# Kernel optimization log

Measured on AMD Instinct MI355X. Metric: run time of the kernel, lower is better.

The kernel has to match this reference:

```python
import jax, jax.numpy as jnp
import numpy as np

EMBED_DIM = 1024
NUM_HEADS = 16
HEAD_DIM = EMBED_DIM // NUM_HEADS


def setup_inputs() -> dict:
    key = jax.random.key(0)
    ks = jax.random.split(key, 11)
    B, S, D = 4, 2048, EMBED_DIM
    s = 1.0 / np.sqrt(D)
    return {
        "query": jax.random.normal(ks[0], (B, S, D), jnp.float32),
        "key": jax.random.normal(ks[1], (B, S, D), jnp.float32),
        "value": jax.random.normal(ks[2], (B, S, D), jnp.float32),
        "Wq": jax.random.normal(ks[3], (D, D), jnp.float32) * s,
        "bq": jnp.zeros((D,), jnp.float32),
        "Wk": jax.random.normal(ks[4], (D, D), jnp.float32) * s,
        "bk": jnp.zeros((D,), jnp.float32),
        "Wv": jax.random.normal(ks[5], (D, D), jnp.float32) * s,
        "bv": jnp.zeros((D,), jnp.float32),
        "Wo": jax.random.normal(ks[6], (D, D), jnp.float32) * s,
        "bo": jnp.zeros((D,), jnp.float32),
    }


def _split_heads(x):
    B, S, D = x.shape
    return x.reshape(B, S, NUM_HEADS, HEAD_DIM).transpose(0, 2, 1, 3)  # (B,H,S,hd)


def reference(query, key, value, Wq, bq, Wk, bk, Wv, bv, Wo, bo):
    q = _split_heads(query @ Wq + bq)
    k = _split_heads(key @ Wk + bk)
    v = _split_heads(value @ Wv + bv)
    # naive scaled dot-product attention: full (B,H,S,S) scores materialized
    scores = jnp.einsum("bhqd,bhkd->bhqk", q, k) / np.sqrt(HEAD_DIM).astype(np.float32)
    attn = jax.nn.softmax(scores, axis=-1)
    ctx = jnp.einsum("bhqk,bhkd->bhqd", attn, v)
    B, H, S, hd = ctx.shape
    ctx = ctx.transpose(0, 2, 1, 3).reshape(B, S, H * hd)
    return ctx @ Wo + bo
```

## Files before the change

### kernel.cpp

```cpp
#include <hip/hip_runtime.h>

typedef unsigned short u16;
typedef unsigned int u32;
typedef _Float16 f16;
typedef __attribute__((ext_vector_type(8))) _Float16 f16x8;
typedef __attribute__((ext_vector_type(4))) float f32x4;
typedef __attribute__((ext_vector_type(4))) u32 u32x4;
typedef __attribute__((ext_vector_type(2))) u32 u32x2;
typedef __attribute__((ext_vector_type(4))) u16 u16x4;

static __device__ __forceinline__ u16 f16r(float f) {
  return __builtin_bit_cast(u16, (_Float16)f);
}
static __device__ __forceinline__ u32 packh(float a, float b) {
  return __builtin_bit_cast(u32, __builtin_amdgcn_cvt_pkrtz(a, b));
}
static __device__ __forceinline__ void gload16(const u16* g, u16* l) {
  __builtin_amdgcn_global_load_lds((const __attribute__((address_space(1))) void*)g,
                                   (__attribute__((address_space(3))) void*)l, 16, 0, 0);
}
static __device__ __forceinline__ void gload16f(const float* g, float* l) {
  __builtin_amdgcn_global_load_lds((const __attribute__((address_space(1))) void*)g,
                                   (__attribute__((address_space(3))) void*)l, 16, 0, 0);
}

__global__ __launch_bounds__(256) void wtrans4_k(
    const float* __restrict__ Wq, const float* __restrict__ Wk,
    const float* __restrict__ Wv, const float* __restrict__ Wo,
    u16* __restrict__ Tq, u16* __restrict__ Tk, u16* __restrict__ Tv, u16* __restrict__ To) {
  int z = blockIdx.z;
  const float* W = z == 0 ? Wq : z == 1 ? Wk : z == 2 ? Wv : Wo;
  u16* WT = z == 0 ? Tq : z == 1 ? Tk : z == 2 ? Tv : To;
  __shared__ float tile[32][33];
  int k0 = blockIdx.x * 32, n0 = blockIdx.y * 32;
  int t = threadIdx.x;
  int r = t >> 3, c = (t & 7) * 4;
  f32x4 v = *(const f32x4*)&W[(size_t)(k0 + r) * 1024 + n0 + c];
  tile[r][c + 0] = v[0]; tile[r][c + 1] = v[1]; tile[r][c + 2] = v[2]; tile[r][c + 3] = v[3];
  __syncthreads();
  int n = n0 + (t >> 3), kbase = k0 + (t & 7) * 4;
  u16x4 o;
#pragma unroll
  for (int j = 0; j < 4; j++) o[j] = f16r(tile[(t & 7) * 4 + j][t >> 3]);
  int nt = n >> 7, row = n & 127;
  int kt = kbase >> 5, lc = (kbase >> 3) & 3, e = kbase & 7;
  int pc = lc ^ ((row >> 1) & 3);
  *(u16x4*)&WT[((size_t)(nt * 32 + kt) * 128 + row) * 32 + pc * 8 + e] = o;
}

__global__ __launch_bounds__(256) void gemm_qkv_k(
    const float* __restrict__ Aq, const float* __restrict__ Ak, const float* __restrict__ Av,
    const u16* __restrict__ Tq, const u16* __restrict__ Tk, const u16* __restrict__ Tv,
    const float* __restrict__ bq, const float* __restrict__ bk, const float* __restrict__ bv,
    u16* __restrict__ Qo, u16* __restrict__ Ko, u16* __restrict__ Vo, float qscale) {
  int z = blockIdx.z;
  const float* A = z == 0 ? Aq : z == 1 ? Ak : Av;
  const u16* BT = z == 0 ? Tq : z == 1 ? Tk : Tv;
  const float* bias = z == 0 ? bq : z == 1 ? bk : bv;
  u16* out = z == 0 ? Qo : z == 1 ? Ko : Vo;
  int vmode = (z == 2);
  float scale = z == 0 ? qscale : 1.0f;

  __shared__ float As[2][128 * 32];
  __shared__ u16 Bs[2][128 * 32];
  int lid = blockIdx.x;
  int xcd = lid & 7, idx = lid >> 3;
  int bx = idx & 7, by = xcd * 8 + (idx >> 3);
  int n0 = bx * 128, m0 = by * 128;
  int tid = threadIdx.x, lane = tid & 63;
  int w = tid >> 6, wr = w >> 1, wc = w & 1;
  int fq = lane & 15, fc = lane >> 4;
  f32x4 acc[4][4] = {};
  const u16* BTb = BT + (size_t)bx * 131072;

  auto stage = [&](int ks, int sel) {
    const float* Ab = A + (size_t)m0 * 1024 + ks * 32;
#pragma unroll
    for (int i = 0; i < 4; i++) {
      int u = (w * 4 + i) * 64 + lane;
      int row = u >> 3, pc = u & 7;
      int koff = (pc ^ (row & 7)) << 2;
      gload16f(Ab + (size_t)row * 1024 + koff, &As[sel][(w * 4 + i) * 256]);
    }
    const u16* Bt = BTb + ks * 4096;
#pragma unroll
    for (int i = 0; i < 2; i++)
      gload16(Bt + (w * 2 + i) * 512 + lane * 8, &Bs[sel][(w * 2 + i) * 512]);
  };

  stage(0, 0);
  stage(1, 1);
  for (int ks = 0; ks < 32; ks++) {
    int cur = ks & 1;
    if (ks < 31) asm volatile("s_waitcnt vmcnt(6)" ::: "memory");
    else         asm volatile("s_waitcnt vmcnt(0)" ::: "memory");
    __builtin_amdgcn_s_barrier();
    __builtin_amdgcn_sched_barrier(0);
    f16x8 af[4], bfv[4];
#pragma unroll
    for (int mi = 0; mi < 4; mi++) {
      int row = wr * 64 + mi * 16 + fq;
      int pc0 = (2 * fc) ^ (row & 7);
      f32x4 x0 = *(const f32x4*)&As[cur][row * 32 + pc0 * 4];
      f32x4 x1 = *(const f32x4*)&As[cur][row * 32 + (pc0 ^ 1) * 4];
      u32x4 pk = {packh(x0[0], x0[1]), packh(x0[2], x0[3]),
                  packh(x1[0], x1[1]), packh(x1[2], x1[3])};
      af[mi] = __builtin_bit_cast(f16x8, pk);
    }
#pragma unroll
    for (int ni = 0; ni < 4; ni++) {
      int row = wc * 64 + ni * 16 + fq;
      bfv[ni] = *(const f16x8*)&Bs[cur][row * 32 + (fc ^ ((row >> 1) & 3)) * 8];
    }
    __builtin_amdgcn_s_setprio(1);
#pragma unroll
    for (int mi = 0; mi < 4; mi++)
#pragma unroll
      for (int ni = 0; ni < 4; ni++)
        acc[mi][ni] = __builtin_amdgcn_mfma_f32_16x16x32_f16(af[mi], bfv[ni], acc[mi][ni], 0, 0, 0);
    __builtin_amdgcn_s_setprio(0);
    __builtin_amdgcn_sched_barrier(0);
    __builtin_amdgcn_s_barrier();
    if (ks < 30) stage(ks + 2, cur);
  }
#pragma unroll
  for (int mi = 0; mi < 4; mi++)
#pragma unroll
    for (int ni = 0; ni < 4; ni++) {
      int n = n0 + wc * 64 + ni * 16 + fq;
      float bs = bias[n];
      int h = n >> 6, d = n & 63;
#pragma unroll
      for (int r = 0; r < 4; r++) {
        int m = m0 + wr * 64 + mi * 16 + fc * 4 + r;
        int b = m >> 11, s = m & 2047;
        float v = (acc[mi][ni][r] + bs) * scale;
        size_t o;
        if (vmode == 0) {
          int t = s >> 4, fqo = s & 15, kco = d >> 5, fco = (d & 31) >> 3, e = d & 7;
          o = (size_t)(b * 16 + h) * 131072 + (size_t)((((t * 2 + kco) * 64) + fco * 16 + fqo) * 8 + e);
        } else {
          int kvc = s >> 5, dt = d >> 4, fqo = d & 15, fco = (s & 31) >> 3, e = s & 7;
          o = (size_t)(b * 16 + h) * 131072 + (size_t)((((kvc * 4 + dt) * 64) + fco * 16 + fqo) * 8 + e);
        }
        out[o] = f16r(v);
      }
    }
}

__global__ __launch_bounds__(256) void gemm_o_k(
    const u16* __restrict__ Ag, const u16* __restrict__ Bg,
    const float* __restrict__ bias, float* __restrict__ out) {
  __shared__ u16 SA[2][8192];
  __shared__ u16 SB[2][8192];
  int lid = blockIdx.x;
  int xcd = lid & 7, idx = lid >> 3;
  int bx = idx & 7, by = xcd * 8 + (idx >> 3);
  int n0 = bx * 128, m0 = by * 128;
  int tid = threadIdx.x, lane = tid & 63;
  int w = tid >> 6, wr = w >> 1, wc = w & 1;
  int fq = lane & 15, fc = lane >> 4;
  f32x4 acc[4][4] = {};

  auto stage = [&](int ks, int sel) {
    size_t at = ((size_t)by * 16 + ks) * 8192;
    size_t bt = ((size_t)bx * 32 + ks * 2) * 4096;
#pragma unroll
    for (int i = 0; i < 4; i++) {
      int ub = (w * 4 + i) * 512;
      gload16(Ag + at + ub + lane * 8, &SA[sel][ub]);
      gload16(Bg + bt + ub + lane * 8, &SB[sel][ub]);
    }
  };

  stage(0, 0);
  stage(1, 1);
  for (int ks = 0; ks < 16; ks++) {
    int cur = ks & 1;
    if (ks < 15) asm volatile("s_waitcnt vmcnt(8)" ::: "memory");
    else         asm volatile("s_waitcnt vmcnt(0)" ::: "memory");
    __builtin_amdgcn_s_barrier();
    __builtin_amdgcn_sched_barrier(0);
#pragma unroll
    for (int kc = 0; kc < 2; kc++) {
      f16x8 ah[4], bh[4];
#pragma unroll
      for (int mi = 0; mi < 4; mi++) {
        int row = wr * 64 + mi * 16 + fq;
        ah[mi] = *(const f16x8*)&SA[cur][row * 64 + (((kc * 4 + fc) ^ (row & 7)) << 3)];
      }
#pragma unroll
      for (int ni = 0; ni < 4; ni++) {
        int row = wc * 64 + ni * 16 + fq;
        bh[ni] = *(const f16x8*)&SB[cur][kc * 4096 + row * 32 + (fc ^ ((row >> 1) & 3)) * 8];
      }
      __builtin_amdgcn_s_setprio(1);
#pragma unroll
      for (int mi = 0; mi < 4; mi++)
#pragma unroll
        for (int ni = 0; ni < 4; ni++)
          acc[mi][ni] = __builtin_amdgcn_mfma_f32_16x16x32_f16(ah[mi], bh[ni], acc[mi][ni], 0, 0, 0);
      __builtin_amdgcn_s_setprio(0);
    }
    __builtin_amdgcn_sched_barrier(0);
    __builtin_amdgcn_s_barrier();
    if (ks < 14) stage(ks + 2, cur);
  }
#pragma unroll
  for (int mi = 0; mi < 4; mi++)
#pragma unroll
    for (int ni = 0; ni < 4; ni++) {
      int n = n0 + wc * 64 + ni * 16 + fq;
      float bs = bias[n];
#pragma unroll
      for (int r = 0; r < 4; r++) {
        int m = m0 + wr * 64 + mi * 16 + fc * 4 + r;
        out[(size_t)m * 1024 + n] = acc[mi][ni][r] + bs;
      }
    }
}

__global__ __launch_bounds__(512) void attn_k(
    const u16* __restrict__ Q, const u16* __restrict__ Kg, const u16* __restrict__ Vg,
    u16* __restrict__ ctx) {
  int lid = blockIdx.x;
  int bh = (lid & 7) * 8 + (lid >> 6);
  int qb = (lid >> 3) & 7;
  int tid = threadIdx.x, lane = tid & 63, w = tid >> 6;
  const u16* Qf = Q + (size_t)bh * 131072;
  const u16* Kf = Kg + (size_t)bh * 131072;
  const u16* Vf = Vg + (size_t)bh * 131072;
  int fq = lane & 15, fc = lane >> 4;
  int le = lane * 8;
  int q0 = qb * 256 + w * 32;

  __shared__ u16 KL[2][4096];
  __shared__ u16 VL[2][4096];
  __shared__ u16 P[8][1152];

  f16x8 qf[2][2];
#pragma unroll
  for (int mi = 0; mi < 2; mi++)
#pragma unroll
    for (int kc = 0; kc < 2; kc++)
      qf[mi][kc] = *(const f16x8*)&Qf[((((q0 + 16 * mi) >> 4) * 2 + kc) << 9) + le];

  f32x4 O[2][4] = {};
  float lrow[2] = {0.f, 0.f};

  auto stage = [&](int tt, int bb) {
    int qo = (w & 3) * 1024;
    if (w < 4) {
      const u16* Kt = Kf + tt * 4096;
      gload16(Kt + qo + le, &KL[bb][qo]);
      gload16(Kt + qo + 512 + le, &KL[bb][qo + 512]);
    } else {
      const u16* Vt = Vf + tt * 4096;
      gload16(Vt + qo + le, &VL[bb][qo]);
      gload16(Vt + qo + 512 + le, &VL[bb][qo + 512]);
    }
  };

  stage(0, 0);
  stage(1, 1);
  for (int t = 0; t < 32; t++) {
    int buf = t & 1;
    if (t < 31) asm volatile("s_waitcnt vmcnt(2)" ::: "memory");
    else        asm volatile("s_waitcnt vmcnt(0)" ::: "memory");
    __builtin_amdgcn_s_barrier();
    __builtin_amdgcn_sched_barrier(0);

    f16x8 kf[8];
#pragma unroll
    for (int c = 0; c < 8; c++) kf[c] = *(const f16x8*)&KL[buf][c * 512 + le];

    f32x4 sc[2][4] = {};
    __builtin_amdgcn_s_setprio(1);
#pragma unroll
    for (int mi = 0; mi < 2; mi++)
#pragma unroll
      for (int sub = 0; sub < 4; sub++)
#pragma unroll
        for (int kc = 0; kc < 2; kc++)
          sc[mi][sub] = __builtin_amdgcn_mfma_f32_16x16x32_f16(kf[sub * 2 + kc], qf[mi][kc],
                                                               sc[mi][sub], 0, 0, 0);
    __builtin_amdgcn_s_setprio(0);

    f16x8 vf[8];
#pragma unroll
    for (int c = 0; c < 8; c++) vf[c] = *(const f16x8*)&VL[buf][c * 512 + le];

#pragma unroll
    for (int mi = 0; mi < 2; mi++) {
      float lloc = 0.f;
#pragma unroll
      for (int sub = 0; sub < 4; sub++) {
        float p0 = __builtin_amdgcn_exp2f(sc[mi][sub][0]);
        float p1 = __builtin_amdgcn_exp2f(sc[mi][sub][1]);
        float p2 = __builtin_amdgcn_exp2f(sc[mi][sub][2]);
        float p3 = __builtin_amdgcn_exp2f(sc[mi][sub][3]);
        lloc += (p0 + p1) + (p2 + p3);
        u32x2 pw = {packh(p0, p1), packh(p2, p3)};
        *(u32x2*)&P[w][fq * 72 + sub * 16 + fc * 4] = pw;
      }
      lloc += __shfl_xor(lloc, 16);
      lloc += __shfl_xor(lloc, 32);
      lrow[mi] += lloc;

      asm volatile("s_waitcnt lgkmcnt(0)" ::: "memory");
      __builtin_amdgcn_sched_barrier(0);
      __builtin_amdgcn_s_setprio(1);
#pragma unroll
      for (int ch = 0; ch < 2; ch++) {
        f16x8 pa = *(const f16x8*)&P[w][fq * 72 + ch * 32 + fc * 8];
#pragma unroll
        for (int db = 0; db < 4; db++)
          O[mi][db] = __builtin_amdgcn_mfma_f32_16x16x32_f16(pa, vf[ch * 4 + db], O[mi][db], 0, 0, 0);
      }
      __builtin_amdgcn_s_setprio(0);
    }

    __builtin_amdgcn_sched_barrier(0);
    __builtin_amdgcn_s_barrier();
    if (t < 30) stage(t + 2, buf);
  }

  int b = bh >> 4, h = bh & 15;
#pragma unroll
  for (int mi = 0; mi < 2; mi++) {
    float linv[4];
#pragma unroll
    for (int r = 0; r < 4; r++) linv[r] = 1.0f / __shfl(lrow[mi], fc * 4 + r);
#pragma unroll
    for (int db = 0; db < 4; db++)
#pragma unroll
      for (int r = 0; r < 4; r++) {
        float v = O[mi][db][r] * linv[r];
        int s = q0 + mi * 16 + fc * 4 + r;
        int mrow = s & 127, mt = b * 16 + (s >> 7);
        int lc = (db * 16 + fq) >> 3, e = fq & 7;
        int pc = lc ^ (mrow & 7);
        size_t o = ((size_t)(mt * 16 + h) * 128 + mrow) * 64 + pc * 8 + e;
        ctx[o] = f16r(v);
      }
  }
}

extern "C" void kernel_launch(void* const* d_in, const int* in_sizes, int n_in,
                              void* d_out, int out_size, void* d_ws, size_t ws_size,
                              hipStream_t stream) {
  const float* query = (const float*)d_in[0];
  const float* key   = (const float*)d_in[1];
  const float* value = (const float*)d_in[2];
  const float* Wq = (const float*)d_in[3];
  const float* bq = (const float*)d_in[4];
  const float* Wk = (const float*)d_in[5];
  const float* bk = (const float*)d_in[6];
  const float* Wv = (const float*)d_in[7];
  const float* bv = (const float*)d_in[8];
  const float* Wo = (const float*)d_in[9];
  const float* bo = (const float*)d_in[10];
  float* out = (float*)d_out;

  char* ws = (char*)d_ws;
  size_t off = 0;
  auto alloc = [&](size_t bytes) {
    char* p = ws + off;
    off += (bytes + 255) & ~(size_t)255;
    return p;
  };
  u16* WqT = (u16*)alloc(1048576 * 2);
  u16* WkT = (u16*)alloc(1048576 * 2);
  u16* WvT = (u16*)alloc(1048576 * 2);
  u16* WoT = (u16*)alloc(1048576 * 2);
  u16* Qbf = (u16*)alloc((size_t)8388608 * 2);
  u16* Kbf = (u16*)alloc((size_t)8388608 * 2);
  u16* ctx = (u16*)alloc((size_t)8388608 * 2);
  u16* Vfb = (u16*)d_out;

  const float QSCALE = 0.125f * 1.44269504f;

  wtrans4_k<<<dim3(32, 32, 4), 256, 0, stream>>>(Wq, Wk, Wv, Wo, WqT, WkT, WvT, WoT);
  gemm_qkv_k<<<dim3(512, 1, 3), 256, 0, stream>>>(query, key, value, WqT, WkT, WvT,
                                                  bq, bk, bv, Qbf, Kbf, Vfb, QSCALE);
  attn_k<<<512, 512, 0, stream>>>(Qbf, Kbf, Vfb, ctx);
  gemm_o_k<<<512, 256, 0, stream>>>(ctx, WoT, bo, out);
}
```

Before: 192.8 us.

## Pre-convert QKV activations to fp16 tiled layout in a fused prep kernel

Adds a prep kernel that converts the fp32 query/key/value inputs into swizzled fp16 tiles with a 64-wide K chunk, alongside the weight transposes, all in one launch. The QKV GEMM then stages fp16 A and B tiles directly through global_load_lds with a BK=64 loop, in the same style as the output projection. Weight tiles move to the same 64-wide swizzle. This drops per-iteration fp32 LDS traffic and in-loop packing but adds an extra pass that reads the inputs once and writes them back at half size, and it reuses the output buffer as scratch.

```diff
diff --git a/kernel.cpp b/kernel.cpp
--- a/kernel.cpp
+++ b/kernel.cpp
@@ -19,50 +19,64 @@
   __builtin_amdgcn_global_load_lds((const __attribute__((address_space(1))) void*)g,
                                    (__attribute__((address_space(3))) void*)l, 16, 0, 0);
 }
-static __device__ __forceinline__ void gload16f(const float* g, float* l) {
-  __builtin_amdgcn_global_load_lds((const __attribute__((address_space(1))) void*)g,
-                                   (__attribute__((address_space(3))) void*)l, 16, 0, 0);
-}
-
-__global__ __launch_bounds__(256) void wtrans4_k(
+
+__global__ __launch_bounds__(256) void prep_k(
+    const float* __restrict__ Aq, const float* __restrict__ Ak, const float* __restrict__ Av,
     const float* __restrict__ Wq, const float* __restrict__ Wk,
     const float* __restrict__ Wv, const float* __restrict__ Wo,
+    u16* __restrict__ Q16, u16* __restrict__ K16, u16* __restrict__ V16,
     u16* __restrict__ Tq, u16* __restrict__ Tk, u16* __restrict__ Tv, u16* __restrict__ To) {
-  int z = blockIdx.z;
-  const float* W = z == 0 ? Wq : z == 1 ? Wk : z == 2 ? Wv : Wo;
-  u16* WT = z == 0 ? Tq : z == 1 ? Tk : z == 2 ? Tv : To;
   __shared__ float tile[32][33];
-  int k0 = blockIdx.x * 32, n0 = blockIdx.y * 32;
-  int t = threadIdx.x;
-  int r = t >> 3, c = (t & 7) * 4;
-  f32x4 v = *(const f32x4*)&W[(size_t)(k0 + r) * 1024 + n0 + c];
-  tile[r][c + 0] = v[0]; tile[r][c + 1] = v[1]; tile[r][c + 2] = v[2]; tile[r][c + 3] = v[3];
-  __syncthreads();
-  int n = n0 + (t >> 3), kbase = k0 + (t & 7) * 4;
-  u16x4 o;
-#pragma unroll
-  for (int j = 0; j < 4; j++) o[j] = f16r(tile[(t & 7) * 4 + j][t >> 3]);
-  int nt = n >> 7, row = n & 127;
-  int kt = kbase >> 5, lc = (kbase >> 3) & 3, e = kbase & 7;
-  int pc = lc ^ ((row >> 1) & 3);
-  *(u16x4*)&WT[((size_t)(nt * 32 + kt) * 128 + row) * 32 + pc * 8 + e] = o;
+  int bid = blockIdx.x;
+  if (bid < 12288) {
+    int z = bid >> 12, blk = bid & 4095;
+    const float* A = z == 0 ? Aq : z == 1 ? Ak : Av;
+    u16* O = z == 0 ? Q16 : z == 1 ? K16 : V16;
+    int id = blk * 256 + threadIdx.x;
+    int m = id >> 7, c = id & 127;
+    f32x4 x0 = *(const f32x4*)&A[(size_t)m * 1024 + c * 8];
+    f32x4 x1 = *(const f32x4*)&A[(size_t)m * 1024 + c * 8 + 4];
+    u32x4 pk = {packh(x0[0], x0[1]), packh(x0[2], x0[3]),
+                packh(x1[0], x1[1]), packh(x1[2], x1[3])};
+    int mt = m >> 7, row = m & 127;
+    int kt = c >> 3, lc = c & 7, pc = lc ^ (row & 7);
+    *(u32x4*)&O[((size_t)(mt * 16 + kt) * 128 + row) * 64 + pc * 8] = pk;
+  } else {
+    int wz = (bid - 12288) >> 10, blk = (bid - 12288) & 1023;
+    const float* W = wz == 0 ? Wq : wz == 1 ? Wk : wz == 2 ? Wv : Wo;
+    u16* WT = wz == 0 ? Tq : wz == 1 ? Tk : wz == 2 ? Tv : To;
+    int k0 = (blk & 31) * 32, n0 = (blk >> 5) * 32;
+    int t = threadIdx.x;
+    int r = t >> 3, c = (t & 7) * 4;
+    f32x4 v = *(const f32x4*)&W[(size_t)(k0 + r) * 1024 + n0 + c];
+    tile[r][c + 0] = v[0]; tile[r][c + 1] = v[1]; tile[r][c + 2] = v[2]; tile[r][c + 3] = v[3];
+    __syncthreads();
+    int n = n0 + (t >> 3), kbase = k0 + (t & 7) * 4;
+    u16x4 o;
+#pragma unroll
+    for (int j = 0; j < 4; j++) o[j] = f16r(tile[(t & 7) * 4 + j][t >> 3]);
+    int nt = n >> 7, row = n & 127;
+    int kt = kbase >> 6, lc = (kbase >> 3) & 7, e = kbase & 7;
+    int pc = lc ^ (row & 7);
+    *(u16x4*)&WT[((size_t)(nt * 16 + kt) * 128 + row) * 64 + pc * 8 + e] = o;
+  }
 }
 
 __global__ __launch_bounds__(256) void gemm_qkv_k(
-    const float* __restrict__ Aq, const float* __restrict__ Ak, const float* __restrict__ Av,
+    const u16* __restrict__ Aq, const u16* __restrict__ Ak, const u16* __restrict__ Av,
     const u16* __restrict__ Tq, const u16* __restrict__ Tk, const u16* __restrict__ Tv,
     const float* __restrict__ bq, const float* __restrict__ bk, const float* __restrict__ bv,
     u16* __restrict__ Qo, u16* __restrict__ Ko, u16* __restrict__ Vo, float qscale) {
   int z = blockIdx.z;
-  const float* A = z == 0 ? Aq : z == 1 ? Ak : Av;
+  const u16* A = z == 0 ? Aq : z == 1 ? Ak : Av;
   const u16* BT = z == 0 ? Tq : z == 1 ? Tk : Tv;
   const float* bias = z == 0 ? bq : z == 1 ? bk : bv;
   u16* out = z == 0 ? Qo : z == 1 ? Ko : Vo;
   int vmode = (z == 2);
   float scale = z == 0 ? qscale : 1.0f;
 
-  __shared__ float As[2][128 * 32];
-  __shared__ u16 Bs[2][128 * 32];
+  __shared__ u16 As[2][8192];
+  __shared__ u16 Bs[2][8192];
   int lid = blockIdx.x;
   int xcd = lid & 7, idx = lid >> 3;
   int bx = idx & 7, by = xcd * 8 + (idx >> 3);
@@ -71,57 +85,52 @@
   int w = tid >> 6, wr = w >> 1, wc = w & 1;
   int fq = lane & 15, fc = lane >> 4;
   f32x4 acc[4][4] = {};
-  const u16* BTb = BT + (size_t)bx * 131072;
+  const u16* Ab = A + (size_t)by * 131072;
+  const u16* Bb = BT + (size_t)bx * 131072;
 
   auto stage = [&](int ks, int sel) {
-    const float* Ab = A + (size_t)m0 * 1024 + ks * 32;
+    const u16* At = Ab + (size_t)ks * 8192;
+    const u16* Bt = Bb + (size_t)ks * 8192;
 #pragma unroll
     for (int i = 0; i < 4; i++) {
-      int u = (w * 4 + i) * 64 + lane;
-      int row = u >> 3, pc = u & 7;
-      int koff = (pc ^ (row & 7)) << 2;
-      gload16f(Ab + (size_t)row * 1024 + koff, &As[sel][(w * 4 + i) * 256]);
-    }
-    const u16* Bt = BTb + ks * 4096;
-#pragma unroll
-    for (int i = 0; i < 2; i++)
-      gload16(Bt + (w * 2 + i) * 512 + lane * 8, &Bs[sel][(w * 2 + i) * 512]);
+      int ub = (w * 4 + i) * 512;
+      gload16(At + ub + lane * 8, &As[sel][ub]);
+      gload16(Bt + ub + lane * 8, &Bs[sel][ub]);
+    }
   };
 
   stage(0, 0);
   stage(1, 1);
-  for (int ks = 0; ks < 32; ks++) {
+  for (int ks = 0; ks < 16; ks++) {
     int cur = ks & 1;
-    if (ks < 31) asm volatile("s_waitcnt vmcnt(6)" ::: "memory");
+    if (ks < 15) asm volatile("s_waitcnt vmcnt(8)" ::: "memory");
     else         asm volatile("s_waitcnt vmcnt(0)" ::: "memory");
     __builtin_amdgcn_s_barrier();
     __builtin_amdgcn_sched_barrier(0);
-    f16x8 af[4], bfv[4];
-#pragma unroll
-    for (int mi = 0; mi < 4; mi++) {
-      int row = wr * 64 + mi * 16 + fq;
-      int pc0 = (2 * fc) ^ (row & 7);
-      f32x4 x0 = *(const f32x4*)&As[cur][row * 32 + pc0 * 4];
-      f32x4 x1 = *(const f32x4*)&As[cur][row * 32 + (pc0 ^ 1) * 4];
-      u32x4 pk = {packh(x0[0], x0[1]), packh(x0[2], x0[3]),
-                  packh(x1[0], x1[1]), packh(x1[2], x1[3])};
-      af[mi] = __builtin_bit_cast(f16x8, pk);
-    }
-#pragma unroll
-    for (int ni = 0; ni < 4; ni++) {
-      int row = wc * 64 + ni * 16 + fq;
-      bfv[ni] = *(const f16x8*)&Bs[cur][row * 32 + (fc ^ ((row >> 1) & 3)) * 8];
-    }
-    __builtin_amdgcn_s_setprio(1);
-#pragma unroll
-    for (int mi = 0; mi < 4; mi++)
-#pragma unroll
-      for (int ni = 0; ni < 4; ni++)
-        acc[mi][ni] = __builtin_amdgcn_mfma_f32_16x16x32_f16(af[mi], bfv[ni], acc[mi][ni], 0, 0, 0);
-    __builtin_amdgcn_s_setprio(0);
-    __builtin_amdgcn_sched_barrier(0);
-    __builtin_amdgcn_s_barrier();
-    if (ks < 30) stage(ks + 2, cur);
+#pragma unroll
+    for (int kc = 0; kc < 2; kc++) {
+      f16x8 af[4], bfv[4];
+#pragma unroll
+      for (int mi = 0; mi < 4; mi++) {
+        int row = wr * 64 + mi * 16 + fq;
+        af[mi] = *(const f16x8*)&As[cur][row * 64 + (((kc * 4 + fc) ^ (row & 7)) << 3)];
+      }
+#pragma unroll
+      for (int ni = 0; ni < 4; ni++) {
+        int row = wc * 64 + ni * 16 + fq;
+        bfv[ni] = *(const f16x8*)&Bs[cur][row * 64 + (((kc * 4 + fc) ^ (row & 7)) << 3)];
+      }
+      __builtin_amdgcn_s_setprio(1);
+#pragma unroll
+      for (int mi = 0; mi < 4; mi++)
+#pragma unroll
+        for (int ni = 0; ni < 4; ni++)
+          acc[mi][ni] = __builtin_amdgcn_mfma_f32_16x16x32_f16(af[mi], bfv[ni], acc[mi][ni], 0, 0, 0);
+      __builtin_amdgcn_s_setprio(0);
+    }
+    __builtin_amdgcn_sched_barrier(0);
+    __builtin_amdgcn_s_barrier();
+    if (ks < 14) stage(ks + 2, cur);
   }
 #pragma unroll
   for (int mi = 0; mi < 4; mi++)
@@ -161,15 +170,17 @@
   int w = tid >> 6, wr = w >> 1, wc = w & 1;
   int fq = lane & 15, fc = lane >> 4;
   f32x4 acc[4][4] = {};
+  const u16* Ab = Ag + (size_t)by * 131072;
+  const u16* Bb = Bg + (size_t)bx * 131072;
 
   auto stage = [&](int ks, int sel) {
-    size_t at = ((size_t)by * 16 + ks) * 8192;
-    size_t bt = ((size_t)bx * 32 + ks * 2) * 4096;
+    const u16* At = Ab + (size_t)ks * 8192;
+    const u16* Bt = Bb + (size_t)ks * 8192;
 #pragma unroll
     for (int i = 0; i < 4; i++) {
       int ub = (w * 4 + i) * 512;
-      gload16(Ag + at + ub + lane * 8, &SA[sel][ub]);
-      gload16(Bg + bt + ub + lane * 8, &SB[sel][ub]);
+      gload16(At + ub + lane * 8, &SA[sel][ub]);
+      gload16(Bt + ub + lane * 8, &SB[sel][ub]);
     }
   };
 
@@ -192,7 +203,7 @@
 #pragma unroll
       for (int ni = 0; ni < 4; ni++) {
         int row = wc * 64 + ni * 16 + fq;
-        bh[ni] = *(const f16x8*)&SB[cur][kc * 4096 + row * 32 + (fc ^ ((row >> 1) & 3)) * 8];
+        bh[ni] = *(const f16x8*)&SB[cur][row * 64 + (((kc * 4 + fc) ^ (row & 7)) << 3)];
       }
       __builtin_amdgcn_s_setprio(1);
 #pragma unroll
@@ -369,19 +380,23 @@
     off += (bytes + 255) & ~(size_t)255;
     return p;
   };
-  u16* WqT = (u16*)alloc(1048576 * 2);
-  u16* WkT = (u16*)alloc(1048576 * 2);
-  u16* WvT = (u16*)alloc(1048576 * 2);
-  u16* WoT = (u16*)alloc(1048576 * 2);
-  u16* Qbf = (u16*)alloc((size_t)8388608 * 2);
-  u16* Kbf = (u16*)alloc((size_t)8388608 * 2);
-  u16* ctx = (u16*)alloc((size_t)8388608 * 2);
-  u16* Vfb = (u16*)d_out;
+  u16* WqT  = (u16*)alloc(1048576 * 2);
+  u16* WkT  = (u16*)alloc(1048576 * 2);
+  u16* WvT  = (u16*)alloc(1048576 * 2);
+  u16* WoT  = (u16*)alloc(1048576 * 2);
+  u16* Aq16 = (u16*)alloc((size_t)8388608 * 2);
+  u16* Ak16 = (u16*)alloc((size_t)8388608 * 2);
+  u16* Qbf  = (u16*)alloc((size_t)8388608 * 2);
+  u16* Kbf  = (u16*)alloc((size_t)8388608 * 2);
+  u16* ctx  = Aq16;
+  u16* Vfb  = (u16*)d_out;
+  u16* Av16 = (u16*)d_out + 8388608;
 
   const float QSCALE = 0.125f * 1.44269504f;
 
-  wtrans4_k<<<dim3(32, 32, 4), 256, 0, stream>>>(Wq, Wk, Wv, Wo, WqT, WkT, WvT, WoT);
-  gemm_qkv_k<<<dim3(512, 1, 3), 256, 0, stream>>>(query, key, value, WqT, WkT, WvT,
+  prep_k<<<16384, 256, 0, stream>>>(query, key, value, Wq, Wk, Wv, Wo,
+                                    Aq16, Ak16, Av16, WqT, WkT, WvT, WoT);
+  gemm_qkv_k<<<dim3(512, 1, 3), 256, 0, stream>>>(Aq16, Ak16, Av16, WqT, WkT, WvT,
                                                   bq, bk, bv, Qbf, Kbf, Vfb, QSCALE);
   attn_k<<<512, 512, 0, stream>>>(Qbf, Kbf, Vfb, ctx);
   gemm_o_k<<<512, 256, 0, stream>>>(ctx, WoT, bo, out);
```

After: 202.8 us. 5.2% more time.
